# Optimization experiments

Measured on AMD Instinct MI355X. Metric: run time of the kernel, lower is better.

## Reference

```python
import jax, jax.numpy as jnp
import numpy as np

CH = 1280
HEADS = 8
HEAD_DIM = 160
INNER = HEADS * HEAD_DIM  # 1280


def setup_inputs() -> dict:
    key = jax.random.key(0)
    ks = jax.random.split(key, 6)
    s = 1.0 / np.sqrt(CH)
    return {
        "hidden_states": jax.random.normal(ks[0], (2, 4096, CH), dtype=jnp.float32),
        "w_q": jax.random.normal(ks[1], (CH, INNER), dtype=jnp.float32) * s,
        "w_k": jax.random.normal(ks[2], (CH, INNER), dtype=jnp.float32) * s,
        "w_v": jax.random.normal(ks[3], (CH, INNER), dtype=jnp.float32) * s,
        "w_out": jax.random.normal(ks[4], (INNER, CH), dtype=jnp.float32) * (1.0 / np.sqrt(INNER)),
        "b_out": jax.random.normal(ks[5], (CH,), dtype=jnp.float32) * 0.01,
    }


def reference(hidden_states, w_q, w_k, w_v, w_out, b_out):
    B, S, C = hidden_states.shape
    scale = 1.0 / np.sqrt(HEAD_DIM)
    # self-attention: context = hidden_states
    q = (hidden_states @ w_q).reshape(B, S, HEADS, HEAD_DIM)
    k = (hidden_states @ w_k).reshape(B, S, HEADS, HEAD_DIM)
    v = (hidden_states @ w_v).reshape(B, S, HEADS, HEAD_DIM)
    # [B, H, S, S] explicit score matrix (matches original non-flash path)
    scores = jnp.einsum("bqhd,bkhd->bhqk", q, k) * scale
    attn = jax.nn.softmax(scores, axis=-1)
    out = jnp.einsum("bhqk,bkhd->bqhd", attn, v).reshape(B, S, INNER)
    return out @ w_out + b_out
```

## Files before the change

### kernel.cpp

```cpp
#include <hip/hip_runtime.h>
#include <hip/hip_bf16.h>
#include <stdint.h>


using bf16x8 = __attribute__((ext_vector_type(8))) short;
using f32x4  = __attribute__((ext_vector_type(4))) float;

__device__ __forceinline__ short f2bf(float f) {
    union { float f; uint32_t u; } v; v.f = f;
    uint32_t r = v.u + 0x7fffu + ((v.u >> 16) & 1u);
    return (short)(r >> 16);
}

__device__ __forceinline__ void async16(const short* g, short* l) {
    __builtin_amdgcn_global_load_lds(
        (const __attribute__((address_space(1))) void*)g,
        (__attribute__((address_space(3))) void*)l, 16, 0, 0);
}

__global__ __launch_bounds__(256) void cast_hs(
    const float* __restrict__ hs, short* __restrict__ out)
{
    int i = (blockIdx.x * 256 + threadIdx.x) * 4;
    float4 v = *(const float4*)&hs[i];
    short4 s; s.x = f2bf(v.x); s.y = f2bf(v.y); s.z = f2bf(v.z); s.w = f2bf(v.w);
    *(short4*)&out[i] = s;
}

__global__ __launch_bounds__(256) void transpose_w(
    const float* __restrict__ w0, const float* __restrict__ w1,
    const float* __restrict__ w2, const float* __restrict__ w3,
    short* __restrict__ wqkvT, short* __restrict__ woutT)
{
    __shared__ float tile[32][33];
    int z = blockIdx.z;
    const float* src = (z == 0) ? w0 : (z == 1) ? w1 : (z == 2) ? w2 : w3;
    short* dst = (z == 3) ? woutT : (wqkvT + (long)z * 1280 * 1280);
    int k0 = blockIdx.x * 32, n0 = blockIdx.y * 32;
    int t = threadIdx.x, r = t >> 5, c = t & 31;
#pragma unroll
    for (int i = 0; i < 4; i++)
        tile[r + i * 8][c] = src[(long)(k0 + r + i * 8) * 1280 + n0 + c];
    __syncthreads();
#pragma unroll
    for (int i = 0; i < 4; i++)
        dst[(long)(n0 + r + i * 8) * 1280 + k0 + c] = f2bf(tile[c][r + i * 8]);
}

__global__ __launch_bounds__(256) void transpose_v(
    const short* __restrict__ v, short* __restrict__ vt)
{
    __shared__ short tile[32][33];
    int s0 = blockIdx.x * 32, d0 = blockIdx.y * 32;
    long bh = blockIdx.z;
    const short* src = v + bh * 4096 * 160;
    short* dst = vt + bh * 160 * 4096;
    int t = threadIdx.x, r = t >> 5, c = t & 31;
#pragma unroll
    for (int i = 0; i < 4; i++)
        tile[r + i * 8][c] = src[(s0 + r + i * 8) * 160 + d0 + c];
    __syncthreads();
#pragma unroll
    for (int i = 0; i < 4; i++)
        dst[(d0 + r + i * 8) * 4096 + s0 + c] = tile[c][r + i * 8];
}

template <int MODE>
__global__ __launch_bounds__(256, 3) void gemm_k(
    const short* __restrict__ A, const short* __restrict__ BT,
    short* __restrict__ q_h, short* __restrict__ k_h, short* __restrict__ v_h,
    float* __restrict__ outp, const float* __restrict__ bias)
{
    __shared__ __align__(16) short A_lds[128 * 64];
    __shared__ __align__(16) short B_lds[128 * 64];

    int t = threadIdx.x, wave = t >> 6, lane = t & 63;
    int quad = lane >> 4, l15 = lane & 15, h7 = l15 & 7;
    int wr = wave >> 1, wc = wave & 1;
    int m0 = blockIdx.y * 128, n0 = blockIdx.x * 128;

    f32x4 acc[4][4] = {};

    for (int kt = 0; kt < 1280; kt += 64) {
        __syncthreads();
#pragma unroll
        for (int i = 0; i < 4; i++) {
            int chunk = wave * 4 + i;
            int c = chunk * 64 + lane;
            int row = c >> 3, j = (c & 7) ^ (row & 7);
            async16(A  + (long)(m0 + row) * 1280 + kt + j * 8, A_lds + chunk * 512);
            async16(BT + (long)(n0 + row) * 1280 + kt + j * 8, B_lds + chunk * 512);
        }
        __syncthreads();

#pragma unroll
        for (int dk = 0; dk < 2; dk++) {
            bf16x8 a[4], b[4];
#pragma unroll
            for (int mi = 0; mi < 4; mi++) {
                int row = wr * 64 + mi * 16 + l15;
                a[mi] = *(const bf16x8*)&A_lds[row * 64 + ((dk * 4 + quad) ^ h7) * 8];
            }
#pragma unroll
            for (int ni = 0; ni < 4; ni++) {
                int row = wc * 64 + ni * 16 + l15;
                b[ni] = *(const bf16x8*)&B_lds[row * 64 + ((dk * 4 + quad) ^ h7) * 8];
            }
#pragma unroll
            for (int mi = 0; mi < 4; mi++)
#pragma unroll
                for (int ni = 0; ni < 4; ni++)
                    acc[mi][ni] = __builtin_amdgcn_mfma_f32_16x16x32_bf16(
                        a[mi], b[ni], acc[mi][ni], 0, 0, 0);
        }
    }

    const float SL2E = 0.07905694150420949f * 1.4426950408889634f;
#pragma unroll
    for (int mi = 0; mi < 4; mi++) {
#pragma unroll
        for (int ni = 0; ni < 4; ni++) {
#pragma unroll
            for (int r = 0; r < 4; r++) {
                int gr = m0 + wr * 64 + mi * 16 + quad * 4 + r;
                int gc = n0 + wc * 64 + ni * 16 + l15;
                float val = acc[mi][ni][r];
                if (MODE == 0) {
                    int which = gc / 1280;
                    int c1 = gc - which * 1280;
                    int hh = c1 / 160, d = c1 - hh * 160;
                    int b_ = gr >> 12, s = gr & 4095;
                    long addr = (((long)(b_ * 8 + hh)) * 4096 + s) * 160 + d;
                    if (which == 0) val *= SL2E;
                    short* dst = (which == 0) ? q_h : (which == 1) ? k_h : v_h;
                    dst[addr] = f2bf(val);
                } else {
                    outp[(long)gr * 1280 + gc] = val + bias[gc];
                }
            }
        }
    }
}

__global__ __launch_bounds__(256, 2) void flash_k(
    const short* __restrict__ q_h, const short* __restrict__ k_h,
    const short* __restrict__ v_t, short* __restrict__ attn_out)
{
    __shared__ __align__(16) short Ks128[64 * 128];
    __shared__ __align__(16) short Ks32 [64 * 32];
    __shared__ __align__(16) short Vs   [176 * 64];
    __shared__ __align__(16) short Ps   [128 * 72];

    int t = threadIdx.x, wave = t >> 6, lane = t & 63;
    int quad = lane >> 4, l15 = lane & 15, h7 = l15 & 7;
    int qt = blockIdx.x;
    long bh = blockIdx.y;
    int b = (int)(bh >> 3), h = (int)(bh & 7);

    bf16x8 qf[2][5];
#pragma unroll
    for (int mi = 0; mi < 2; mi++) {
        const short* qg = q_h + (bh * 4096 + qt * 128 + wave * 32 + mi * 16 + l15) * 160;
#pragma unroll
        for (int dk = 0; dk < 5; dk++)
            qf[mi][dk] = *(const bf16x8*)&qg[dk * 32 + quad * 8];
    }
    {
        short v1 = (t < 16) ? (short)0x3F80 : (short)0;
        short4 s4 = { v1, v1, v1, v1 };
        *(short4*)&Vs[160 * 64 + t * 4] = s4;
    }

    f32x4 o[2][11] = {};

    for (int k0 = 0; k0 < 4096; k0 += 64) {
        __syncthreads();
        const short* kg = k_h + (bh * 4096 + k0) * 160;
#pragma unroll
        for (int i = 0; i < 4; i++) {
            int chunk = wave * 4 + i;
            int c = chunk * 64 + lane;
            int row = c >> 4, j = (c & 15) ^ (row & 7);
            async16(kg + row * 160 + j * 8, Ks128 + chunk * 512);
        }
        {
            int row = wave * 16 + (lane >> 2);
            int j = (lane & 3) ^ (row & 3);
            async16(kg + row * 160 + 128 + j * 8, Ks32 + wave * 512);
        }
#pragma unroll
        for (int i = 0; i < 5; i++) {
            int chunk = wave * 5 + i;
            int c = chunk * 64 + lane;
            int row = c >> 3, j = (c & 7) ^ (row & 7);
            async16(v_t + (bh * 160 + row) * 4096 + k0 + j * 8, Vs + chunk * 512);
        }
        __syncthreads();

#pragma unroll
        for (int nt = 0; nt < 4; nt++) {
            f32x4 s0 = {}, s1 = {};
#pragma unroll
            for (int dk = 0; dk < 4; dk++) {
                bf16x8 bk = *(const bf16x8*)
                    &Ks128[(nt * 16 + l15) * 128 + ((dk * 4 + quad) ^ h7) * 8];
                s0 = __builtin_amdgcn_mfma_f32_16x16x32_bf16(qf[0][dk], bk, s0, 0, 0, 0);
                s1 = __builtin_amdgcn_mfma_f32_16x16x32_bf16(qf[1][dk], bk, s1, 0, 0, 0);
            }
            {
                bf16x8 bk = *(const bf16x8*)
                    &Ks32[(nt * 16 + l15) * 32 + ((quad ^ (l15 & 3)) * 8)];
                s0 = __builtin_amdgcn_mfma_f32_16x16x32_bf16(qf[0][4], bk, s0, 0, 0, 0);
                s1 = __builtin_amdgcn_mfma_f32_16x16x32_bf16(qf[1][4], bk, s1, 0, 0, 0);
            }
#pragma unroll
            for (int r = 0; r < 4; r++) {
                int pr0 = (wave * 32 + quad * 4 + r) * 72 + nt * 16 + l15;
                Ps[pr0]            = f2bf(exp2f(s0[r] - 16.f));
                Ps[pr0 + 16 * 72]  = f2bf(exp2f(s1[r] - 16.f));
            }
        }

#pragma unroll
        for (int ks = 0; ks < 2; ks++) {
            bf16x8 ap0 = *(const bf16x8*)&Ps[(wave * 32 + l15) * 72 + ks * 32 + quad * 8];
            bf16x8 ap1 = *(const bf16x8*)&Ps[(wave * 32 + 16 + l15) * 72 + ks * 32 + quad * 8];
#pragma unroll
            for (int ct = 0; ct < 11; ct++) {
                int row = ct * 16 + l15;
                bf16x8 bv = *(const bf16x8*)&Vs[row * 64 + (((ks * 4 + quad) ^ (row & 7)) * 8)];
                o[0][ct] = __builtin_amdgcn_mfma_f32_16x16x32_bf16(ap0, bv, o[0][ct], 0, 0, 0);
                o[1][ct] = __builtin_amdgcn_mfma_f32_16x16x32_bf16(ap1, bv, o[1][ct], 0, 0, 0);
            }
        }
    }

#pragma unroll
    for (int mi = 0; mi < 2; mi++) {
        float inv[4];
#pragma unroll
        for (int r = 0; r < 4; r++)
            inv[r] = 1.0f / __shfl(o[mi][10][r], (lane & 48));
#pragma unroll
        for (int ct = 0; ct < 10; ct++)
#pragma unroll
            for (int r = 0; r < 4; r++) {
                int gr = b * 4096 + qt * 128 + wave * 32 + mi * 16 + quad * 4 + r;
                int gc = h * 160 + ct * 16 + l15;
                attn_out[(long)gr * 1280 + gc] = f2bf(o[mi][ct][r] * inv[r]);
            }
    }
}

extern "C" void kernel_launch(void* const* d_in, const int* in_sizes, int n_in,
                              void* d_out, int out_size, void* d_ws, size_t ws_size,
                              hipStream_t stream)
{
    const float* hs = (const float*)d_in[0];
    const float* wq = (const float*)d_in[1];
    const float* wk = (const float*)d_in[2];
    const float* wv = (const float*)d_in[3];
    const float* wo = (const float*)d_in[4];
    const float* bo = (const float*)d_in[5];
    float* out = (float*)d_out;

    char* ws = (char*)d_ws;
    short* wqkvT = (short*)(ws + 0);
    short* woutT = (short*)(ws + 9830400);
    short* q_h   = (short*)(ws + 13107200);
    short* k_h   = (short*)(ws + 34078720);
    short* v_t   = (short*)(ws + 55050240);
    short* v_h   = (short*)(ws + 76021760);
    short* attn  = v_h;
    short* hs_bf = v_t;

    cast_hs<<<10240, 256, 0, stream>>>(hs, hs_bf);
    transpose_w<<<dim3(40, 40, 4), 256, 0, stream>>>(wq, wk, wv, wo, wqkvT, woutT);
    gemm_k<0><<<dim3(30, 64), 256, 0, stream>>>(hs_bf, wqkvT, q_h, k_h, v_h,
                                                nullptr, nullptr);
    transpose_v<<<dim3(128, 5, 16), 256, 0, stream>>>(v_h, v_t);
    flash_k<<<dim3(32, 16), 256, 0, stream>>>(q_h, k_h, v_t, attn);
    gemm_k<1><<<dim3(10, 64), 256, 0, stream>>>(attn, woutT, nullptr, nullptr,
                                                nullptr, out, bo);
}
```

Baseline: 474.0 us.

## Double-buffer K tiles, overlap V load with QK, compute row sums in registers

The flash attention loop now prefetches the next K tile into a second LDS buffer. The current V tile loads while the QK^T MFMAs and exp run, and a partial vmcnt wait lets the K prefetch stay in flight. The softmax denominator no longer comes from an extra ones-column in V, which cost an 11th output tile of MFMAs. Instead each lane sums the fp32 probabilities and a shuffle reduction combines them at the end. LDS use rises with the extra K buffer, and the last iteration prefetches one tile past the head's K range.

```diff
diff --git a/kernel.cpp b/kernel.cpp
--- a/kernel.cpp
+++ b/kernel.cpp
@@ -146,9 +146,9 @@
     const short* __restrict__ q_h, const short* __restrict__ k_h,
     const short* __restrict__ v_t, short* __restrict__ attn_out)
 {
-    __shared__ __align__(16) short Ks128[64 * 128];
-    __shared__ __align__(16) short Ks32 [64 * 32];
-    __shared__ __align__(16) short Vs   [176 * 64];
+    __shared__ __align__(16) short Ks128[2][64 * 128];
+    __shared__ __align__(16) short Ks32 [2][64 * 32];
+    __shared__ __align__(16) short Vs   [160 * 64];
     __shared__ __align__(16) short Ps   [128 * 72];
 
     int t = threadIdx.x, wave = t >> 6, lane = t & 63;
@@ -157,6 +157,8 @@
     long bh = blockIdx.y;
     int b = (int)(bh >> 3), h = (int)(bh & 7);
 
+    const short* kg_base = k_h + bh * 4096 * 160;
+
     bf16x8 qf[2][5];
 #pragma unroll
     for (int mi = 0; mi < 2; mi++) {
@@ -165,37 +167,47 @@
         for (int dk = 0; dk < 5; dk++)
             qf[mi][dk] = *(const bf16x8*)&qg[dk * 32 + quad * 8];
     }
+
+#pragma unroll
+    for (int i = 0; i < 4; i++) {
+        int chunk = wave * 4 + i;
+        int c = chunk * 64 + lane;
+        int row = c >> 4, j = (c & 15) ^ (row & 7);
+        async16(kg_base + row * 160 + j * 8, &Ks128[0][chunk * 512]);
+    }
     {
-        short v1 = (t < 16) ? (short)0x3F80 : (short)0;
-        short4 s4 = { v1, v1, v1, v1 };
-        *(short4*)&Vs[160 * 64 + t * 4] = s4;
-    }
-
-    f32x4 o[2][11] = {};
+        int row = wave * 16 + (lane >> 2);
+        int j = (lane & 3) ^ (row & 3);
+        async16(kg_base + row * 160 + 128 + j * 8, &Ks32[0][wave * 512]);
+    }
+
+    f32x4 o[2][10] = {};
+    float l_part[2][4] = {};
+    __syncthreads();
 
     for (int k0 = 0; k0 < 4096; k0 += 64) {
-        __syncthreads();
-        const short* kg = k_h + (bh * 4096 + k0) * 160;
-#pragma unroll
-        for (int i = 0; i < 4; i++) {
-            int chunk = wave * 4 + i;
-            int c = chunk * 64 + lane;
-            int row = c >> 4, j = (c & 15) ^ (row & 7);
-            async16(kg + row * 160 + j * 8, Ks128 + chunk * 512);
-        }
-        {
-            int row = wave * 16 + (lane >> 2);
-            int j = (lane & 3) ^ (row & 3);
-            async16(kg + row * 160 + 128 + j * 8, Ks32 + wave * 512);
-        }
+        int pb = (k0 >> 6) & 1;
+
 #pragma unroll
         for (int i = 0; i < 5; i++) {
             int chunk = wave * 5 + i;
             int c = chunk * 64 + lane;
             int row = c >> 3, j = (c & 7) ^ (row & 7);
-            async16(v_t + (bh * 160 + row) * 4096 + k0 + j * 8, Vs + chunk * 512);
-        }
-        __syncthreads();
+            async16(v_t + (bh * 160 + row) * 4096 + k0 + j * 8, &Vs[chunk * 512]);
+        }
+        {
+            const short* kg = kg_base + (k0 + 64) * 160;
+#pragma unroll
+            for (int i = 0; i < 4; i++) {
+                int chunk = wave * 4 + i;
+                int c = chunk * 64 + lane;
+                int row = c >> 4, j = (c & 15) ^ (row & 7);
+                async16(kg + row * 160 + j * 8, &Ks128[pb ^ 1][chunk * 512]);
+            }
+            int row = wave * 16 + (lane >> 2);
+            int j = (lane & 3) ^ (row & 3);
+            async16(kg + row * 160 + 128 + j * 8, &Ks32[pb ^ 1][wave * 512]);
+        }
 
 #pragma unroll
         for (int nt = 0; nt < 4; nt++) {
@@ -203,44 +215,57 @@
 #pragma unroll
             for (int dk = 0; dk < 4; dk++) {
                 bf16x8 bk = *(const bf16x8*)
-                    &Ks128[(nt * 16 + l15) * 128 + ((dk * 4 + quad) ^ h7) * 8];
+                    &Ks128[pb][(nt * 16 + l15) * 128 + ((dk * 4 + quad) ^ h7) * 8];
                 s0 = __builtin_amdgcn_mfma_f32_16x16x32_bf16(qf[0][dk], bk, s0, 0, 0, 0);
                 s1 = __builtin_amdgcn_mfma_f32_16x16x32_bf16(qf[1][dk], bk, s1, 0, 0, 0);
             }
             {
                 bf16x8 bk = *(const bf16x8*)
-                    &Ks32[(nt * 16 + l15) * 32 + ((quad ^ (l15 & 3)) * 8)];
+                    &Ks32[pb][(nt * 16 + l15) * 32 + ((quad ^ (l15 & 3)) * 8)];
                 s0 = __builtin_amdgcn_mfma_f32_16x16x32_bf16(qf[0][4], bk, s0, 0, 0, 0);
                 s1 = __builtin_amdgcn_mfma_f32_16x16x32_bf16(qf[1][4], bk, s1, 0, 0, 0);
             }
 #pragma unroll
             for (int r = 0; r < 4; r++) {
+                float p0 = exp2f(s0[r] - 16.f);
+                float p1 = exp2f(s1[r] - 16.f);
                 int pr0 = (wave * 32 + quad * 4 + r) * 72 + nt * 16 + l15;
-                Ps[pr0]            = f2bf(exp2f(s0[r] - 16.f));
-                Ps[pr0 + 16 * 72]  = f2bf(exp2f(s1[r] - 16.f));
-            }
-        }
+                Ps[pr0]           = f2bf(p0);
+                Ps[pr0 + 16 * 72] = f2bf(p1);
+                l_part[0][r] += p0;
+                l_part[1][r] += p1;
+            }
+        }
+
+        asm volatile("s_waitcnt vmcnt(5)" ::: "memory");
+        asm volatile("s_barrier" ::: "memory");
 
 #pragma unroll
         for (int ks = 0; ks < 2; ks++) {
             bf16x8 ap0 = *(const bf16x8*)&Ps[(wave * 32 + l15) * 72 + ks * 32 + quad * 8];
             bf16x8 ap1 = *(const bf16x8*)&Ps[(wave * 32 + 16 + l15) * 72 + ks * 32 + quad * 8];
 #pragma unroll
-            for (int ct = 0; ct < 11; ct++) {
+            for (int ct = 0; ct < 10; ct++) {
                 int row = ct * 16 + l15;
                 bf16x8 bv = *(const bf16x8*)&Vs[row * 64 + (((ks * 4 + quad) ^ (row & 7)) * 8)];
                 o[0][ct] = __builtin_amdgcn_mfma_f32_16x16x32_bf16(ap0, bv, o[0][ct], 0, 0, 0);
                 o[1][ct] = __builtin_amdgcn_mfma_f32_16x16x32_bf16(ap1, bv, o[1][ct], 0, 0, 0);
             }
         }
+
+        __syncthreads();
     }
 
 #pragma unroll
     for (int mi = 0; mi < 2; mi++) {
         float inv[4];
 #pragma unroll
-        for (int r = 0; r < 4; r++)
-            inv[r] = 1.0f / __shfl(o[mi][10][r], (lane & 48));
+        for (int r = 0; r < 4; r++) {
+            float l = l_part[mi][r];
+#pragma unroll
+            for (int m = 1; m < 16; m <<= 1) l += __shfl_xor(l, m);
+            inv[r] = 1.0f / l;
+        }
 #pragma unroll
         for (int ct = 0; ct < 10; ct++)
 #pragma unroll
```

After: 493.4 us. +4.1%, slower.
